# Optimization experiments

Measured on AMD Instinct MI355X. Metric: run time of the kernel, lower is better.

## Reference

```python
import jax, jax.numpy as jnp
import numpy as np

WS = (8, 8)   # window size
SS = (4, 4)   # shift size
NH = 3        # num heads


def _attn_mask(pad_H, pad_W):
    """Standard Swin shifted-window attention mask, shape (nW, L, L)."""
    img = np.zeros((pad_H, pad_W), dtype=np.int32)
    cnt = 0
    for hs in (slice(0, -WS[0]), slice(-WS[0], -SS[0]), slice(-SS[0], None)):
        for ws_ in (slice(0, -WS[1]), slice(-WS[1], -SS[1]), slice(-SS[1], None)):
            img[hs, ws_] = cnt
            cnt += 1
    nH, nW = pad_H // WS[0], pad_W // WS[1]
    m = img.reshape(nH, WS[0], nW, WS[1]).transpose(0, 2, 1, 3).reshape(nH * nW, WS[0] * WS[1])
    diff = m[:, None, :] - m[:, :, None]
    return jnp.asarray(np.where(diff != 0, -100.0, 0.0).astype(np.float32))


def setup_inputs() -> dict:
    key = jax.random.key(0)
    ks = jax.random.split(key, 6)
    B, H, W, C = 16, 128, 128, 96
    L = WS[0] * WS[1]
    return {
        "x": jax.random.normal(ks[0], (B, H, W, C), jnp.float32),
        "qkv_w": jax.random.normal(ks[1], (3 * C, C), jnp.float32) * 0.05,
        "qkv_b": jax.random.normal(ks[2], (3 * C,), jnp.float32) * 0.05,
        "proj_w": jax.random.normal(ks[3], (C, C), jnp.float32) * 0.05,
        "proj_b": jax.random.normal(ks[4], (C,), jnp.float32) * 0.05,
        "rel_bias": jax.random.normal(ks[5], (NH, L, L), jnp.float32) * 0.05,
    }


def reference(x, qkv_w, qkv_b, proj_w, proj_b, rel_bias):
    B, H, W, C = x.shape
    pad_b = (WS[0] - H % WS[0]) % WS[0]
    pad_r = (WS[1] - W % WS[1]) % WS[1]
    x = jnp.pad(x, ((0, 0), (0, pad_b), (0, pad_r), (0, 0)))
    pad_H, pad_W = H + pad_b, W + pad_r
    ss = [0 if WS[0] >= pad_H else SS[0], 0 if WS[1] >= pad_W else SS[1]]
    shifted = sum(ss) > 0
    if shifted:
        x = jnp.roll(x, (-ss[0], -ss[1]), axis=(1, 2))
    nH, nW = pad_H // WS[0], pad_W // WS[1]
    num_win = nH * nW
    L = WS[0] * WS[1]
    d = C // NH
    # window partition -> (B*nW, L, C)
    xw = x.reshape(B, nH, WS[0], nW, WS[1], C).transpose(0, 1, 3, 2, 4, 5)
    xw = xw.reshape(B * num_win, L, C)
    # qkv projection
    qkv = xw @ qkv_w.T + qkv_b                       # (BnW, L, 3C)
    qkv = qkv.reshape(B * num_win, L, 3, NH, d).transpose(2, 0, 3, 1, 4)
    q, k, v = qkv[0], qkv[1], qkv[2]                 # (BnW, NH, L, d)
    q = q * (d ** -0.5)
    attn = jnp.einsum("whqd,whkd->whqk", q, k)       # (BnW, NH, L, L)
    attn = attn + rel_bias[None]
    if shifted:
        mask = _attn_mask(pad_H, pad_W)              # (nW, L, L)
        attn = attn.reshape(B, num_win, NH, L, L) + mask[None, :, None]
        attn = attn.reshape(B * num_win, NH, L, L)
    attn = jax.nn.softmax(attn, axis=-1)
    out = jnp.einsum("whqk,whkd->whqd", attn, v)     # (BnW, NH, L, d)
    out = out.transpose(0, 2, 1, 3).reshape(B * num_win, L, C)
    out = out @ proj_w.T + proj_b
    # un-window
    out = out.reshape(B, nH, nW, WS[0], WS[1], C).transpose(0, 1, 3, 2, 4, 5)
    out = out.reshape(B, pad_H, pad_W, C)
    if shifted:
        out = jnp.roll(out, (ss[0], ss[1]), axis=(1, 2))
    return out[:, :H, :W, :]
```

## Files before the change

kernel.cpp:

```cpp
#include <hip/hip_runtime.h>


typedef __attribute__((ext_vector_type(8))) short short8;
typedef __attribute__((ext_vector_type(4))) float f32x4;

#define XST 104
#define QST 40
#define VST 72
#define PST 72

#define WS_QKVW 0
#define WS_PROJW 27648
#define WS_QKVB_BYTES 73728
#define WS_PROJB_BYTES 74880

__device__ __forceinline__ unsigned short f2b(float f) {
    union { float f; unsigned u; } v; v.f = f;
    unsigned r = v.u + 0x7fffu + ((v.u >> 16) & 1u);
    return (unsigned short)(r >> 16);
}

__global__ void prep_weights(const float* __restrict__ qkv_w,
                             const float* __restrict__ qkv_b,
                             const float* __restrict__ proj_w,
                             const float* __restrict__ proj_b,
                             void* __restrict__ ws)
{
    unsigned short* wsh = (unsigned short*)ws;
    float* fqb = (float*)((char*)ws + WS_QKVB_BYTES);
    float* fpb = (float*)((char*)ws + WS_PROJB_BYTES);
    const float qs = 0.17677669529663687f;

    int idx = blockIdx.x * 256 + threadIdx.x;
    if (idx < 27648) {
        int col = idx / 96;
        float v = qkv_w[idx];
        if (col < 96) v *= qs;
        wsh[WS_QKVW + idx] = f2b(v);
    } else if (idx < 36864) {
        wsh[WS_PROJW + (idx - 27648)] = f2b(proj_w[idx - 27648]);
    } else if (idx < 37152) {
        int col = idx - 36864;
        float v = qkv_b[col];
        if (col < 96) v *= qs;
        fqb[col] = v;
    } else if (idx < 37248) {
        fpb[idx - 37152] = proj_b[idx - 37152];
    }
}

__global__ __launch_bounds__(256, 3) void swin_mfma(
    const float* __restrict__ x,
    const float* __restrict__ rel_bias,
    const void* __restrict__ ws,
    float* __restrict__ out)
{
    const unsigned short* wqkv  = (const unsigned short*)ws + WS_QKVW;
    const unsigned short* wproj = (const unsigned short*)ws + WS_PROJW;
    const float* wqkvb = (const float*)((const char*)ws + WS_QKVB_BYTES);
    const float* wprjb = (const float*)((const char*)ws + WS_PROJB_BYTES);

    __shared__ __align__(16) unsigned short xs[64 * XST];
    __shared__ __align__(16) unsigned short kb[3 * 64 * QST];
    __shared__ __align__(16) unsigned short vt[3 * 32 * VST];
    __shared__ __align__(16) unsigned short pb[64 * PST];

    const int t    = threadIdx.x;
    const int wv   = t >> 6;
    const int lane = t & 63;
    const int quad = lane >> 4;
    const int l16  = lane & 15;
    const int m0   = wv * 16;

    const int blk = blockIdx.x;
    const int bb  = blk >> 8;
    const int win = blk & 255;
    const int wh  = win >> 4, ww = win & 15;

    for (int idx = t; idx < 1536; idx += 256) {
        int row = idx / 24;
        int c4  = idx - row * 24;
        int r = row >> 3, c = row & 7;
        int gh = (wh * 8 + r + 4) & 127;
        int gw = (ww * 8 + c + 4) & 127;
        float4 v = *(const float4*)&x[(((bb * 128 + gh) * 128 + gw) * 96) + c4 * 4];
        ushort4 pk;
        pk.x = f2b(v.x); pk.y = f2b(v.y); pk.z = f2b(v.z); pk.w = f2b(v.w);
        *(ushort4*)&xs[row * XST + c4 * 4] = pk;
    }
    __syncthreads();

    short8 af[4][3];
    #pragma unroll
    for (int mt = 0; mt < 4; ++mt)
        #pragma unroll
        for (int ks = 0; ks < 3; ++ks)
            af[mt][ks] = *(const short8*)&xs[(mt * 16 + l16) * XST + ks * 32 + quad * 8];
    __syncthreads();

    for (int nt = wv; nt < 18; nt += 4) {
        const int n0 = nt * 16;
        float bias = wqkvb[n0 + l16];
        f32x4 acc[4];
        #pragma unroll
        for (int mt = 0; mt < 4; ++mt) acc[mt] = (f32x4){bias, bias, bias, bias};
        #pragma unroll
        for (int ks = 0; ks < 3; ++ks) {
            short8 bf = *(const short8*)&wqkv[(n0 + l16) * 96 + ks * 32 + quad * 8];
            #pragma unroll
            for (int mt = 0; mt < 4; ++mt)
                acc[mt] = __builtin_amdgcn_mfma_f32_16x16x32_bf16(af[mt][ks], bf, acc[mt], 0, 0, 0);
        }
        if (nt < 6) {
            int col = n0 + l16;
            #pragma unroll
            for (int mt = 0; mt < 4; ++mt)
                #pragma unroll
                for (int r = 0; r < 4; ++r)
                    xs[(mt * 16 + quad * 4 + r) * XST + col] = f2b(acc[mt][r]);
        } else if (nt < 12) {
            int col = n0 - 96 + l16; int h = col >> 5; int d = col & 31;
            #pragma unroll
            for (int mt = 0; mt < 4; ++mt)
                #pragma unroll
                for (int r = 0; r < 4; ++r)
                    kb[(h * 64 + mt * 16 + quad * 4 + r) * QST + d] = f2b(acc[mt][r]);
        } else {
            int col = n0 - 192 + l16; int h = col >> 5; int d = col & 31;
            #pragma unroll
            for (int mt = 0; mt < 4; ++mt) {
                ushort4 pk;
                pk.x = f2b(acc[mt][0]); pk.y = f2b(acc[mt][1]);
                pk.z = f2b(acc[mt][2]); pk.w = f2b(acc[mt][3]);
                *(ushort4*)&vt[(h * 32 + d) * VST + mt * 16 + quad * 4] = pk;
            }
        }
    }
    __syncthreads();

    {
        const bool bh = (wh == 15), bw = (ww == 15);
        int qrr[4], qcc[4];
        #pragma unroll
        for (int r = 0; r < 4; ++r) {
            int tok = m0 + quad * 4 + r;
            qrr[r] = bh ? (((tok >> 3) < 4) ? 1 : 2) : 0;
            qcc[r] = bw ? (((tok & 7) < 4) ? 1 : 2) : 0;
        }

        for (int h = 0; h < 3; ++h) {
            short8 qa = *(const short8*)&xs[(m0 + l16) * XST + h * 32 + quad * 8];
            f32x4 s[4];
            #pragma unroll
            for (int nt = 0; nt < 4; ++nt) {
                short8 kf = *(const short8*)&kb[(h * 64 + nt * 16 + l16) * QST + quad * 8];
                f32x4 z = (f32x4){0.f, 0.f, 0.f, 0.f};
                s[nt] = __builtin_amdgcn_mfma_f32_16x16x32_bf16(qa, kf, z, 0, 0, 0);
            }
            float rsum[4] = {0.f, 0.f, 0.f, 0.f};
            #pragma unroll
            for (int nt = 0; nt < 4; ++nt) {
                int jcol = nt * 16 + l16;
                int jrr = bh ? (((jcol >> 3) < 4) ? 1 : 2) : 0;
                int jcc = bw ? (((jcol & 7) < 4) ? 1 : 2) : 0;
                #pragma unroll
                for (int r = 0; r < 4; ++r) {
                    float bias = rel_bias[(h * 64 + m0 + quad * 4 + r) * 64 + jcol];
                    float mv = ((jrr != qrr[r]) || (jcc != qcc[r])) ? -100.f : 0.f;
                    float e = __expf(s[nt][r] + bias + mv);
                    rsum[r] += e;
                    pb[(m0 + quad * 4 + r) * PST + jcol] = f2b(e);
                }
            }
            #pragma unroll
            for (int r = 0; r < 4; ++r) {
                float sv = rsum[r];
                sv += __shfl_xor(sv, 1);
                sv += __shfl_xor(sv, 2);
                sv += __shfl_xor(sv, 4);
                sv += __shfl_xor(sv, 8);
                rsum[r] = 1.0f / sv;
            }
            f32x4 o0 = (f32x4){0.f, 0.f, 0.f, 0.f};
            f32x4 o1 = o0;
            #pragma unroll
            for (int kk = 0; kk < 2; ++kk) {
                short8 pa = *(const short8*)&pb[(m0 + l16) * PST + kk * 32 + quad * 8];
                short8 v0 = *(const short8*)&vt[(h * 32 + l16) * VST + kk * 32 + quad * 8];
                short8 v1 = *(const short8*)&vt[(h * 32 + 16 + l16) * VST + kk * 32 + quad * 8];
                o0 = __builtin_amdgcn_mfma_f32_16x16x32_bf16(pa, v0, o0, 0, 0, 0);
                o1 = __builtin_amdgcn_mfma_f32_16x16x32_bf16(pa, v1, o1, 0, 0, 0);
            }
            #pragma unroll
            for (int r = 0; r < 4; ++r) {
                xs[(m0 + quad * 4 + r) * XST + h * 32 + l16]      = f2b(o0[r] * rsum[r]);
                xs[(m0 + quad * 4 + r) * XST + h * 32 + 16 + l16] = f2b(o1[r] * rsum[r]);
            }
        }
    }
    __syncthreads();

    {
        short8 pa[3];
        #pragma unroll
        for (int ks = 0; ks < 3; ++ks)
            pa[ks] = *(const short8*)&xs[(m0 + l16) * XST + ks * 32 + quad * 8];

        int rowbase[4];
        #pragma unroll
        for (int r = 0; r < 4; ++r) {
            int tok = m0 + quad * 4 + r;
            int tr = tok >> 3, tc = tok & 7;
            int gh = (wh * 8 + tr + 4) & 127;
            int gw = (ww * 8 + tc + 4) & 127;
            rowbase[r] = ((bb * 128 + gh) * 128 + gw) * 96;
        }
        #pragma unroll
        for (int nt = 0; nt < 6; ++nt) {
            const int n0 = nt * 16;
            float bias = wprjb[n0 + l16];
            f32x4 acc = (f32x4){bias, bias, bias, bias};
            #pragma unroll
            for (int ks = 0; ks < 3; ++ks) {
                short8 bf = *(const short8*)&wproj[(n0 + l16) * 96 + ks * 32 + quad * 8];
                acc = __builtin_amdgcn_mfma_f32_16x16x32_bf16(pa[ks], bf, acc, 0, 0, 0);
            }
            #pragma unroll
            for (int r = 0; r < 4; ++r)
                out[rowbase[r] + n0 + l16] = acc[r];
        }
    }
}

extern "C" void kernel_launch(void* const* d_in, const int* in_sizes, int n_in,
                              void* d_out, int out_size, void* d_ws, size_t ws_size,
                              hipStream_t stream) {
    const float* x        = (const float*)d_in[0];
    const float* qkv_w    = (const float*)d_in[1];
    const float* qkv_b    = (const float*)d_in[2];
    const float* proj_w   = (const float*)d_in[3];
    const float* proj_b   = (const float*)d_in[4];
    const float* rel_bias = (const float*)d_in[5];
    float* out = (float*)d_out;

    hipLaunchKernelGGL(prep_weights, dim3(146), dim3(256), 0, stream,
                       qkv_w, qkv_b, proj_w, proj_b, d_ws);
    hipLaunchKernelGGL(swin_mfma, dim3(4096), dim3(256), 0, stream,
                       x, rel_bias, (const void*)d_ws, out);
}
```

Baseline: 242.8 us.

## Compute transposed attention scores in registers and drop P shared-memory round trip

Swaps the MFMA operands so each lane holds one query's scores across keys. The row sum then needs only two cross-lane shuffles, and the normalized probabilities are repacked into the PV operand with shuffles instead of being staged through an LDS buffer. K in shared memory is stored with an XOR swizzle instead of padding, and a transposed copy of rel_bias is prepared in the workspace for coalesced loads. Mask computation is skipped for interior windows, and launch bounds rise to 4 blocks per CU, which adds register pressure and extra shuffle work.

Result: faster. 235.0 us (-3.2%).

```diff
diff --git a/kernel.cpp b/kernel.cpp
--- a/kernel.cpp
+++ b/kernel.cpp
@@ -5,14 +5,14 @@
 typedef __attribute__((ext_vector_type(4))) float f32x4;
 
 #define XST 104
-#define QST 40
 #define VST 72
-#define PST 72
 
 #define WS_QKVW 0
 #define WS_PROJW 27648
 #define WS_QKVB_BYTES 73728
 #define WS_PROJB_BYTES 74880
+#define WS_BIAST_BYTES 75776
+#define WS_TOTAL_BYTES (WS_BIAST_BYTES + 3 * 64 * 64 * 4)
 
 __device__ __forceinline__ unsigned short f2b(float f) {
     union { float f; unsigned u; } v; v.f = f;
@@ -20,15 +20,21 @@
     return (unsigned short)(r >> 16);
 }
 
+__device__ __forceinline__ unsigned pack2(float a, float b) {
+    return (unsigned)f2b(a) | ((unsigned)f2b(b) << 16);
+}
+
 __global__ void prep_weights(const float* __restrict__ qkv_w,
                              const float* __restrict__ qkv_b,
                              const float* __restrict__ proj_w,
                              const float* __restrict__ proj_b,
-                             void* __restrict__ ws)
+                             const float* __restrict__ rel_bias,
+                             void* __restrict__ ws, int do_bias)
 {
     unsigned short* wsh = (unsigned short*)ws;
     float* fqb = (float*)((char*)ws + WS_QKVB_BYTES);
     float* fpb = (float*)((char*)ws + WS_PROJB_BYTES);
+    float* fbt = (float*)((char*)ws + WS_BIAST_BYTES);
     const float qs = 0.17677669529663687f;
 
     int idx = blockIdx.x * 256 + threadIdx.x;
@@ -46,12 +52,19 @@
         fqb[col] = v;
     } else if (idx < 37248) {
         fpb[idx - 37152] = proj_b[idx - 37152];
-    }
-}
-
-__global__ __launch_bounds__(256, 3) void swin_mfma(
+    } else if (do_bias && idx < 49536) {
+        int i2 = idx - 37248;
+        int h = i2 >> 12;
+        int rem = i2 & 4095;
+        int k = rem >> 6, q = rem & 63;
+        fbt[i2] = rel_bias[(h * 64 + q) * 64 + k];
+    }
+}
+
+__global__ __launch_bounds__(256, 4) void swin_mfma(
     const float* __restrict__ x,
     const float* __restrict__ rel_bias,
+    const float* __restrict__ biasT,
     const void* __restrict__ ws,
     float* __restrict__ out)
 {
@@ -61,9 +74,8 @@
     const float* wprjb = (const float*)((const char*)ws + WS_PROJB_BYTES);
 
     __shared__ __align__(16) unsigned short xs[64 * XST];
-    __shared__ __align__(16) unsigned short kb[3 * 64 * QST];
+    __shared__ __align__(16) unsigned short kb[3 * 64 * 32];
     __shared__ __align__(16) unsigned short vt[3 * 32 * VST];
-    __shared__ __align__(16) unsigned short pb[64 * PST];
 
     const int t    = threadIdx.x;
     const int wv   = t >> 6;
@@ -119,20 +131,24 @@
                 for (int r = 0; r < 4; ++r)
                     xs[(mt * 16 + quad * 4 + r) * XST + col] = f2b(acc[mt][r]);
         } else if (nt < 12) {
-            int col = n0 - 96 + l16; int h = col >> 5; int d = col & 31;
+            int col = n0 - 96 + l16; int hh = col >> 5; int d = col & 31;
+            int dch = d >> 3, dlo = d & 7;
             #pragma unroll
             for (int mt = 0; mt < 4; ++mt)
                 #pragma unroll
-                for (int r = 0; r < 4; ++r)
-                    kb[(h * 64 + mt * 16 + quad * 4 + r) * QST + d] = f2b(acc[mt][r]);
+                for (int r = 0; r < 4; ++r) {
+                    int row = hh * 64 + mt * 16 + quad * 4 + r;
+                    int c = ((dch ^ ((row >> 1) & 3)) << 3) + dlo;
+                    kb[row * 32 + c] = f2b(acc[mt][r]);
+                }
         } else {
-            int col = n0 - 192 + l16; int h = col >> 5; int d = col & 31;
+            int col = n0 - 192 + l16; int hh = col >> 5; int d = col & 31;
             #pragma unroll
             for (int mt = 0; mt < 4; ++mt) {
                 ushort4 pk;
                 pk.x = f2b(acc[mt][0]); pk.y = f2b(acc[mt][1]);
                 pk.z = f2b(acc[mt][2]); pk.w = f2b(acc[mt][3]);
-                *(ushort4*)&vt[(h * 32 + d) * VST + mt * 16 + quad * 4] = pk;
+                *(ushort4*)&vt[(hh * 32 + d) * VST + mt * 16 + quad * 4] = pk;
             }
         }
     }
@@ -140,71 +156,88 @@
 
     {
         const bool bh = (wh == 15), bw = (ww == 15);
-        int qrr[4], qcc[4];
-        #pragma unroll
-        for (int r = 0; r < 4; ++r) {
-            int tok = m0 + quad * 4 + r;
-            qrr[r] = bh ? (((tok >> 3) < 4) ? 1 : 2) : 0;
-            qcc[r] = bw ? (((tok & 7) < 4) ? 1 : 2) : 0;
-        }
+        const bool edge = bh || bw;
+        const int qtok = m0 + l16;
+        const int qrr = bh ? (((qtok >> 3) < 4) ? 1 : 2) : 0;
+        const int qcc = bw ? (((qtok & 7) < 4) ? 1 : 2) : 0;
 
         for (int h = 0; h < 3; ++h) {
             short8 qa = *(const short8*)&xs[(m0 + l16) * XST + h * 32 + quad * 8];
             f32x4 s[4];
             #pragma unroll
             for (int nt = 0; nt < 4; ++nt) {
-                short8 kf = *(const short8*)&kb[(h * 64 + nt * 16 + l16) * QST + quad * 8];
+                int rowk = h * 64 + nt * 16 + l16;
+                short8 kf = *(const short8*)&kb[rowk * 32 + ((quad ^ ((rowk >> 1) & 3)) << 3)];
                 f32x4 z = (f32x4){0.f, 0.f, 0.f, 0.f};
-                s[nt] = __builtin_amdgcn_mfma_f32_16x16x32_bf16(qa, kf, z, 0, 0, 0);
-            }
-            float rsum[4] = {0.f, 0.f, 0.f, 0.f};
+                s[nt] = __builtin_amdgcn_mfma_f32_16x16x32_bf16(kf, qa, z, 0, 0, 0);
+            }
+            float p[4][4];
+            float rs = 0.f;
             #pragma unroll
             for (int nt = 0; nt < 4; ++nt) {
-                int jcol = nt * 16 + l16;
-                int jrr = bh ? (((jcol >> 3) < 4) ? 1 : 2) : 0;
-                int jcc = bw ? (((jcol & 7) < 4) ? 1 : 2) : 0;
                 #pragma unroll
                 for (int r = 0; r < 4; ++r) {
-                    float bias = rel_bias[(h * 64 + m0 + quad * 4 + r) * 64 + jcol];
-                    float mv = ((jrr != qrr[r]) || (jcc != qcc[r])) ? -100.f : 0.f;
-                    float e = __expf(s[nt][r] + bias + mv);
-                    rsum[r] += e;
-                    pb[(m0 + quad * 4 + r) * PST + jcol] = f2b(e);
+                    int ktok = nt * 16 + quad * 4 + r;
+                    float bv = biasT ? biasT[(h * 64 + ktok) * 64 + qtok]
+                                     : rel_bias[(h * 64 + qtok) * 64 + ktok];
+                    float arg = s[nt][r] + bv;
+                    if (edge) {
+                        int krr = bh ? (((ktok >> 3) < 4) ? 1 : 2) : 0;
+                        int kcc = bw ? (((ktok & 7) < 4) ? 1 : 2) : 0;
+                        if (krr != qrr || kcc != qcc) arg -= 100.f;
+                    }
+                    float e = __expf(arg);
+                    p[nt][r] = e;
+                    rs += e;
                 }
             }
-            #pragma unroll
-            for (int r = 0; r < 4; ++r) {
-                float sv = rsum[r];
-                sv += __shfl_xor(sv, 1);
-                sv += __shfl_xor(sv, 2);
-                sv += __shfl_xor(sv, 4);
-                sv += __shfl_xor(sv, 8);
-                rsum[r] = 1.0f / sv;
-            }
+            rs += __shfl_xor(rs, 16);
+            rs += __shfl_xor(rs, 32);
+            float rinv = 1.0f / rs;
+
+            unsigned w2[4][2];
+            #pragma unroll
+            for (int nt = 0; nt < 4; ++nt) {
+                w2[nt][0] = pack2(p[nt][0] * rinv, p[nt][1] * rinv);
+                w2[nt][1] = pack2(p[nt][2] * rinv, p[nt][3] * rinv);
+            }
+            short8 pa[2];
+            #pragma unroll
+            for (int kk = 0; kk < 2; ++kk) {
+                union { unsigned u[4]; short8 s8; } uw;
+                #pragma unroll
+                for (int w = 0; w < 4; ++w) {
+                    int src = (2 * (quad & 1) + (w >> 1)) * 16 + l16;
+                    int lo = __shfl((int)w2[2 * kk][w & 1], src);
+                    int hi = __shfl((int)w2[2 * kk + 1][w & 1], src);
+                    uw.u[w] = (quad & 2) ? (unsigned)hi : (unsigned)lo;
+                }
+                pa[kk] = uw.s8;
+            }
+
             f32x4 o0 = (f32x4){0.f, 0.f, 0.f, 0.f};
             f32x4 o1 = o0;
             #pragma unroll
             for (int kk = 0; kk < 2; ++kk) {
-                short8 pa = *(const short8*)&pb[(m0 + l16) * PST + kk * 32 + quad * 8];
                 short8 v0 = *(const short8*)&vt[(h * 32 + l16) * VST + kk * 32 + quad * 8];
                 short8 v1 = *(const short8*)&vt[(h * 32 + 16 + l16) * VST + kk * 32 + quad * 8];
-                o0 = __builtin_amdgcn_mfma_f32_16x16x32_bf16(pa, v0, o0, 0, 0, 0);
-                o1 = __builtin_amdgcn_mfma_f32_16x16x32_bf16(pa, v1, o1, 0, 0, 0);
+                o0 = __builtin_amdgcn_mfma_f32_16x16x32_bf16(pa[kk], v0, o0, 0, 0, 0);
+                o1 = __builtin_amdgcn_mfma_f32_16x16x32_bf16(pa[kk], v1, o1, 0, 0, 0);
             }
             #pragma unroll
             for (int r = 0; r < 4; ++r) {
-                xs[(m0 + quad * 4 + r) * XST + h * 32 + l16]      = f2b(o0[r] * rsum[r]);
-                xs[(m0 + quad * 4 + r) * XST + h * 32 + 16 + l16] = f2b(o1[r] * rsum[r]);
+                xs[(m0 + quad * 4 + r) * XST + h * 32 + l16]      = f2b(o0[r]);
+                xs[(m0 + quad * 4 + r) * XST + h * 32 + 16 + l16] = f2b(o1[r]);
             }
         }
     }
     __syncthreads();
 
     {
-        short8 pa[3];
+        short8 pja[3];
         #pragma unroll
         for (int ks = 0; ks < 3; ++ks)
-            pa[ks] = *(const short8*)&xs[(m0 + l16) * XST + ks * 32 + quad * 8];
+            pja[ks] = *(const short8*)&xs[(m0 + l16) * XST + ks * 32 + quad * 8];
 
         int rowbase[4];
         #pragma unroll
@@ -223,7 +256,7 @@
             #pragma unroll
             for (int ks = 0; ks < 3; ++ks) {
                 short8 bf = *(const short8*)&wproj[(n0 + l16) * 96 + ks * 32 + quad * 8];
-                acc = __builtin_amdgcn_mfma_f32_16x16x32_bf16(pa[ks], bf, acc, 0, 0, 0);
+                acc = __builtin_amdgcn_mfma_f32_16x16x32_bf16(pja[ks], bf, acc, 0, 0, 0);
             }
             #pragma unroll
             for (int r = 0; r < 4; ++r)
@@ -243,8 +276,12 @@
     const float* rel_bias = (const float*)d_in[5];
     float* out = (float*)d_out;
 
-    hipLaunchKernelGGL(prep_weights, dim3(146), dim3(256), 0, stream,
-                       qkv_w, qkv_b, proj_w, proj_b, d_ws);
+    const float* biasT = nullptr;
+    if (ws_size >= (size_t)WS_TOTAL_BYTES)
+        biasT = (const float*)((const char*)d_ws + WS_BIAST_BYTES);
+
+    hipLaunchKernelGGL(prep_weights, dim3(194), dim3(256), 0, stream,
+                       qkv_w, qkv_b, proj_w, proj_b, rel_bias, d_ws, biasT ? 1 : 0);
     hipLaunchKernelGGL(swin_mfma, dim3(4096), dim3(256), 0, stream,
-                       x, rel_bias, (const void*)d_ws, out);
-}
+                       x, rel_bias, biasT, (const void*)d_ws, out);
+}
```
